# Optimization experiments

Hardware: AMD Instinct MI355X
Metric: run time of the kernel (lower is better)

## Reference

```python
import jax, jax.numpy as jnp
import numpy as np

B, L = 8, 896
D_MODEL, N_HEAD, D_HEAD, D_INNER = 320, 10, 32, 1280
LN_EPS = 1e-5


def layernorm(x, g, b):
    mu = jnp.mean(x, axis=-1, keepdims=True)
    var = jnp.mean(jnp.square(x - mu), axis=-1, keepdims=True)
    return (x - mu) * jax.lax.rsqrt(var + LN_EPS) * g + b


def setup_inputs() -> dict:
    key = jax.random.key(0)
    ks = jax.random.split(key, 8)
    w = lambda k, shape: (jax.random.normal(k, shape, jnp.float32) * 0.02)
    return {
        "Z": jax.random.normal(ks[0], (B, L, D_MODEL), jnp.float32),
        "D": jax.random.uniform(ks[1], (B, L, L), jnp.float32),  # nonneg sq-distance bias
        "new_mask": jnp.zeros((B, L, L), jnp.float32),           # additive mask (0 = keep)
        "mask": jnp.ones((B, L, L), jnp.float32),                # multiplicative validity mask
        "gamma": jnp.ones((4, 4), jnp.float32),
        "w_qkv": w(ks[2], (D_MODEL, 3 * D_MODEL)),
        "b_qkv": jnp.zeros((3 * D_MODEL,), jnp.float32),
        "w_o": w(ks[3], (D_MODEL, D_MODEL)),
        "ln1_g": jnp.ones((D_MODEL,), jnp.float32),
        "ln1_b": jnp.zeros((D_MODEL,), jnp.float32),
        "ln2_g": jnp.ones((D_MODEL,), jnp.float32),
        "ln2_b": jnp.zeros((D_MODEL,), jnp.float32),
        "w1": w(ks[4], (D_MODEL, D_INNER)),
        "b1": jnp.zeros((D_INNER,), jnp.float32),
        "w2": w(ks[5], (D_INNER, D_MODEL)),
        "b2": jnp.zeros((D_MODEL,), jnp.float32),
        "N": 128, "M": 256, "P": 512,
    }


def reference(Z, D, new_mask, mask, gamma, w_qkv, b_qkv, w_o,
              ln1_g, ln1_b, ln2_g, ln2_b, w1, b1, w2, b2, N, M, P):
    bsz, n_elem, _ = Z.shape
    sqrtd = np.sqrt(D_HEAD).astype(np.float32)

    # per-pair type bias: segment ids 0=atom,1=bond,2=triplet (use_quad=False)
    seg = jnp.concatenate([
        jnp.zeros((N,), jnp.int32),
        jnp.ones((M,), jnp.int32),
        jnp.full((P,), 2, jnp.int32),
    ])  # [L]
    gamma_mask = gamma[seg[:, None], seg[None, :]]  # [L, L]

    inp = Z
    Zn = layernorm(Z, ln1_g, ln1_b)
    qkv = (Zn @ w_qkv + b_qkv).reshape(bsz, n_elem, N_HEAD, 3 * D_HEAD)
    Z2, Z3, Z4 = jnp.split(qkv, 3, axis=3)  # each [b, L, h, d]

    # scores [b, h, n, m]
    scores = jnp.einsum('bnhd,bmhd->bhnm', Z3, Z4) / sqrtd
    W = -(gamma_mask[None] * D)[:, None] + scores + new_mask[:, None]
    W = jax.nn.softmax(W, axis=3) * mask[:, None]

    attn_out = jnp.einsum('bhnm,bmhd->bnhd', W, Z2).reshape(bsz, n_elem, D_MODEL)
    attn_out = jax.nn.leaky_relu(attn_out, 0.01) @ w_o  # o_net has no bias
    Z_res = attn_out + inp

    Zn2 = layernorm(Z_res, ln2_g, ln2_b)
    out = jax.nn.relu(Zn2 @ w1 + b1) @ w2 + b2 + Z_res
    return out
```

## Files before the change

kernel.cpp:

```cpp
#include <hip/hip_runtime.h>

#define BB 8
#define LLEN 896
#define DMODEL 320
#define NHEAD 10
#define DHEAD 32
#define DINNER 1280
#define ROWS (BB*LLEN)

typedef float f32x4 __attribute__((ext_vector_type(4)));
typedef float f32x16 __attribute__((ext_vector_type(16)));
typedef __bf16 bf16x8 __attribute__((ext_vector_type(8)));
typedef short s16x8 __attribute__((ext_vector_type(8)));

__device__ __forceinline__ float bf2f(unsigned short u) {
    union { unsigned int i; float f; } x;
    x.i = ((unsigned int)u) << 16;
    return x.f;
}
__device__ __forceinline__ unsigned short f2bf(float f) {
    unsigned int u = __float_as_uint(f);
    u += 0x7FFF + ((u >> 16) & 1);
    return (unsigned short)(u >> 16);
}

#define GLOAD16(g, l)                                                              \
    __builtin_amdgcn_global_load_lds(                                              \
        (const __attribute__((address_space(1))) void*)(g),                        \
        (__attribute__((address_space(3))) void*)(__attribute__((address_space(3))) char*)(l), \
        16, 0, 0)

__global__ __launch_bounds__(256) void transpose_bf16(const float* __restrict__ src,
                                                      unsigned short* __restrict__ dst,
                                                      int R, int C) {
    __shared__ float tile[32][33];
    int c0 = blockIdx.x * 32;
    int r0 = blockIdx.y * 32;
    int tx = threadIdx.x & 31, ty = threadIdx.x >> 5;
#pragma unroll
    for (int k = 0; k < 4; ++k) {
        int yy = ty + 8 * k;
        tile[yy][tx] = src[(size_t)(r0 + yy) * C + c0 + tx];
    }
    __syncthreads();
#pragma unroll
    for (int k = 0; k < 4; ++k) {
        int yy = ty + 8 * k;
        dst[(size_t)(c0 + yy) * R + r0 + tx] = f2bf(tile[tx][yy]);
    }
}

__global__ __launch_bounds__(256) void prepass(const float* __restrict__ D,
                                               const float* __restrict__ nm,
                                               const float* __restrict__ mk,
                                               const float* __restrict__ gamma,
                                               unsigned int* __restrict__ combo) {
    __shared__ unsigned int tile[32][33];
    int mt = blockIdx.x, m0 = mt * 32;
    int n0 = blockIdx.y * 32;
    int b = blockIdx.z;
    int sn = (n0 < 128) ? 0 : (n0 < 384) ? 1 : 2;
    int sm = (m0 < 128) ? 0 : (m0 < 384) ? 1 : 2;
    float g = gamma[sn * 4 + sm];
    int tx = threadIdx.x & 31, ty = threadIdx.x >> 5;
#pragma unroll
    for (int k = 0; k < 4; ++k) {
        int nl = ty + 8 * k;
        size_t idx = ((size_t)b * LLEN + n0 + nl) * LLEN + m0 + tx;
        float bias = -g * D[idx] + nm[idx];
        tile[nl][tx] = (unsigned int)f2bf(bias) | ((unsigned int)f2bf(mk[idx]) << 16);
    }
    __syncthreads();
#pragma unroll
    for (int k = 0; k < 4; ++k) {
        int nl = ty + 8 * k;
        combo[(((size_t)b * 28 + mt) * LLEN + n0 + nl) * 32 + tx] = tile[nl][tx];
    }
}

__global__ __launch_bounds__(256) void vt_kernel(const unsigned short* __restrict__ qkv,
                                                 unsigned short* __restrict__ Vt) {
    __shared__ unsigned short tile[32][33];
    int mt = blockIdx.x, h = blockIdx.y, b = blockIdx.z;
    int tx = threadIdx.x & 31, ty = threadIdx.x >> 5;
#pragma unroll
    for (int k = 0; k < 4; ++k) {
        int ml = ty + 8 * k;
        tile[ml][tx] = qkv[((size_t)(b * LLEN) + mt * 32 + ml) * 960 + h * 96 + tx];
    }
    __syncthreads();
#pragma unroll
    for (int k = 0; k < 4; ++k) {
        int d = ty + 8 * k;
        Vt[(((size_t)b * NHEAD + h) * 32 + d) * LLEN + mt * 32 + tx] = tile[tx][d];
    }
}

__global__ __launch_bounds__(320) void ln_kernel(const float* __restrict__ x,
                                                 const float* __restrict__ g,
                                                 const float* __restrict__ bia,
                                                 unsigned short* __restrict__ y) {
    int row = blockIdx.x;
    int t = threadIdx.x;
    float v = x[(size_t)row * DMODEL + t];
    float s = v;
#pragma unroll
    for (int o = 1; o < 64; o <<= 1) s += __shfl_xor(s, o, 64);
    __shared__ float red[10];
    int w = t >> 6;
    if ((t & 63) == 0) red[w] = s;
    __syncthreads();
    float mu = (red[0] + red[1] + red[2] + red[3] + red[4]) * (1.0f / DMODEL);
    float d = v - mu;
    float s2 = d * d;
#pragma unroll
    for (int o = 1; o < 64; o <<= 1) s2 += __shfl_xor(s2, o, 64);
    if ((t & 63) == 0) red[5 + w] = s2;
    __syncthreads();
    float var = (red[5] + red[6] + red[7] + red[8] + red[9]) * (1.0f / DMODEL);
    float inv = rsqrtf(var + 1e-5f);
    y[(size_t)row * DMODEL + t] = f2bf(d * inv * g[t] + bia[t]);
}

template <int EPI>
__global__ __launch_bounds__(256) void gemm_bt(const unsigned short* __restrict__ A,
                                               const unsigned short* __restrict__ BT,
                                               const float* __restrict__ bias,
                                               const float* __restrict__ resid,
                                               void* __restrict__ outv,
                                               int M, int N, int K) {
    __shared__ unsigned short As[128][64];
    __shared__ unsigned short Bs[64][64];
    int tid = threadIdx.x;
    int m0 = blockIdx.x * 128;
    int n0 = blockIdx.y * 64;
    int wid = tid >> 6, l = tid & 63;
    int wr = wid >> 1, wc = wid & 1;
    int lr = l & 15, lh = l >> 4;
    int srow = tid >> 3;
    int scol = (tid & 7) * 8;
    int wlds = (tid >> 6) * 1024;

    f32x4 acc[4][2];
#pragma unroll
    for (int mi = 0; mi < 4; ++mi)
#pragma unroll
        for (int ni = 0; ni < 2; ++ni) acc[mi][ni] = (f32x4){0.f, 0.f, 0.f, 0.f};

    for (int k0 = 0; k0 < K; k0 += 64) {
        __syncthreads();
#pragma unroll
        for (int i = 0; i < 4; ++i)
            GLOAD16(&A[(size_t)(m0 + i * 32 + srow) * K + k0 + scol],
                    (char*)&As[0][0] + i * 4096 + wlds);
#pragma unroll
        for (int i = 0; i < 2; ++i)
            GLOAD16(&BT[(size_t)(n0 + i * 32 + srow) * K + k0 + scol],
                    (char*)&Bs[0][0] + i * 4096 + wlds);
        __syncthreads();
#pragma unroll
        for (int kk = 0; kk < 2; ++kk) {
            bf16x8 b0 = *(const bf16x8*)&Bs[wc * 32 + lr][kk * 32 + lh * 8];
            bf16x8 b1 = *(const bf16x8*)&Bs[wc * 32 + 16 + lr][kk * 32 + lh * 8];
#pragma unroll
            for (int mi = 0; mi < 4; ++mi) {
                bf16x8 a = *(const bf16x8*)&As[wr * 64 + mi * 16 + lr][kk * 32 + lh * 8];
                acc[mi][0] = __builtin_amdgcn_mfma_f32_16x16x32_bf16(a, b0, acc[mi][0], 0, 0, 0);
                acc[mi][1] = __builtin_amdgcn_mfma_f32_16x16x32_bf16(a, b1, acc[mi][1], 0, 0, 0);
            }
        }
    }

    unsigned short* outb = (unsigned short*)outv;
    float* outf = (float*)outv;
#pragma unroll
    for (int mi = 0; mi < 4; ++mi)
#pragma unroll
        for (int ni = 0; ni < 2; ++ni) {
            int col = n0 + wc * 32 + ni * 16 + lr;
            float bv = (EPI != 1) ? bias[col] : 0.f;
#pragma unroll
            for (int j = 0; j < 4; ++j) {
                int row = m0 + wr * 64 + mi * 16 + lh * 4 + j;
                float v = acc[mi][ni][j];
                if (EPI == 0 || EPI == 2 || EPI == 3) v += bv;
                if (EPI == 2) v = fmaxf(v, 0.0f);
                if (EPI == 1 || EPI == 3) v += resid[(size_t)row * N + col];
                if (EPI == 0 || EPI == 2) outb[(size_t)row * N + col] = f2bf(v);
                else outf[(size_t)row * N + col] = v;
            }
        }
}

__global__ __launch_bounds__(320) void attn_mfma(const unsigned short* __restrict__ qkv,
                                                 const unsigned short* __restrict__ Vt,
                                                 const unsigned int* __restrict__ combo,
                                                 unsigned short* __restrict__ attn) {
    int tid = threadIdx.x;
    int h = blockIdx.y * 5 + (tid >> 6);
    int l = tid & 63;
    int c = l & 31;
    int hi = l >> 5;
    int nt = blockIdx.x % 28;
    int b = blockIdx.x / 28;
    int n0 = nt * 32;

    size_t qbase = ((size_t)(b * LLEN + n0 + c)) * 960 + h * 96 + 32 + hi * 8;
    bf16x8 qB0 = *(const bf16x8*)&qkv[qbase];
    bf16x8 qB1 = *(const bf16x8*)&qkv[qbase + 16];

    f32x16 oacc = {0.f,0.f,0.f,0.f,0.f,0.f,0.f,0.f,0.f,0.f,0.f,0.f,0.f,0.f,0.f,0.f};
    float lsum = 0.f;

    const unsigned int* cbase = combo + ((size_t)b * 28 * LLEN + n0 + c) * 32;
    size_t kbase = (size_t)b * LLEN * 960 + h * 96 + 64 + hi * 8;
    const unsigned short* vrow = Vt + (((size_t)b * NHEAD + h) * 32 + c) * LLEN;

    for (int mt = 0; mt < 28; ++mt) {
        size_t krow = kbase + (size_t)(mt * 32 + c) * 960;
        bf16x8 kA0 = *(const bf16x8*)&qkv[krow];
        bf16x8 kA1 = *(const bf16x8*)&qkv[krow + 16];
        f32x16 sacc = {0.f,0.f,0.f,0.f,0.f,0.f,0.f,0.f,0.f,0.f,0.f,0.f,0.f,0.f,0.f,0.f};
        sacc = __builtin_amdgcn_mfma_f32_32x32x16_bf16(kA0, qB0, sacc, 0, 0, 0);
        sacc = __builtin_amdgcn_mfma_f32_32x32x16_bf16(kA1, qB1, sacc, 0, 0, 0);

        const unsigned int* cp = cbase + (size_t)mt * (LLEN * 32);
        int4 x4[4];
#pragma unroll
        for (int g = 0; g < 4; ++g) x4[g] = *(const int4*)&cp[8 * g + 4 * hi];

        float p[16];
#pragma unroll
        for (int r = 0; r < 16; ++r) {
            unsigned int cm = ((const unsigned int*)x4)[(r >> 2) * 4 + (r & 3)];
            float bias = bf2f((unsigned short)(cm & 0xffffu));
            float mk = bf2f((unsigned short)(cm >> 16));
            float s = fmaf(sacc[r], 0.17677669529663687f, bias);
            float e = __expf(s);
            lsum += e;
            p[r] = e * mk;
        }

        unsigned int u[8], x[8];
#pragma unroll
        for (int j = 0; j < 8; ++j) {
            union { __bf16 h2[2]; unsigned int w; } pk;
            pk.h2[0] = (__bf16)p[2 * j];
            pk.h2[1] = (__bf16)p[2 * j + 1];
            u[j] = pk.w;
            x[j] = (unsigned int)__shfl_xor((int)u[j], 32, 64);
        }
        union { unsigned int w[4]; bf16x8 v; } a1, a2;
        if (hi == 0) {
            a1.w[0] = u[0]; a1.w[1] = u[1]; a1.w[2] = x[0]; a1.w[3] = x[1];
            a2.w[0] = u[4]; a2.w[1] = u[5]; a2.w[2] = x[4]; a2.w[3] = x[5];
        } else {
            a1.w[0] = x[2]; a1.w[1] = x[3]; a1.w[2] = u[2]; a1.w[3] = u[3];
            a2.w[0] = x[6]; a2.w[1] = x[7]; a2.w[2] = u[6]; a2.w[3] = u[7];
        }

        bf16x8 v1 = *(const bf16x8*)&vrow[mt * 32 + hi * 8];
        bf16x8 v2 = *(const bf16x8*)&vrow[mt * 32 + 16 + hi * 8];
        oacc = __builtin_amdgcn_mfma_f32_32x32x16_bf16(a1.v, v1, oacc, 0, 0, 0);
        oacc = __builtin_amdgcn_mfma_f32_32x32x16_bf16(a2.v, v2, oacc, 0, 0, 0);
    }

    lsum += __shfl_xor(lsum, 32, 64);
    float invs = 1.0f / lsum;
#pragma unroll
    for (int r = 0; r < 16; ++r) {
        int n = (r & 3) + 8 * (r >> 2) + 4 * hi;
        float o = oacc[r] * __shfl(invs, n, 64);
        o = (o >= 0.f) ? o : 0.01f * o;
        attn[((size_t)(b * LLEN + n0 + n)) * DMODEL + h * DHEAD + c] = f2bf(o);
    }
}

extern "C" void kernel_launch(void* const* d_in, const int* in_sizes, int n_in,
                              void* d_out, int out_size, void* d_ws, size_t ws_size,
                              hipStream_t stream) {
    const float* Z     = (const float*)d_in[0];
    const float* Dm    = (const float*)d_in[1];
    const float* nmask = (const float*)d_in[2];
    const float* mask  = (const float*)d_in[3];
    const float* gamma = (const float*)d_in[4];
    const float* w_qkv = (const float*)d_in[5];
    const float* b_qkv = (const float*)d_in[6];
    const float* w_o   = (const float*)d_in[7];
    const float* ln1g  = (const float*)d_in[8];
    const float* ln1b  = (const float*)d_in[9];
    const float* ln2g  = (const float*)d_in[10];
    const float* ln2b  = (const float*)d_in[11];
    const float* w1    = (const float*)d_in[12];
    const float* b1    = (const float*)d_in[13];
    const float* w2    = (const float*)d_in[14];
    const float* b2    = (const float*)d_in[15];

    char* ws = (char*)d_ws;
    unsigned short* Zn    = (unsigned short*)(ws + 0);
    unsigned short* qkv   = (unsigned short*)(ws + 4587520);
    unsigned short* attn  = (unsigned short*)(ws + 18350080);
    float*          Zres  = (float*)(ws + 22937600);
    unsigned short* Zn2   = (unsigned short*)(ws + 32112640);
    unsigned short* Hbuf  = (unsigned short*)(ws + 36700160);
    unsigned short* wqkvT = (unsigned short*)(ws + 55050240);
    unsigned short* woT   = (unsigned short*)(ws + 55664640);
    unsigned short* w1T   = (unsigned short*)(ws + 55869440);
    unsigned short* w2T   = (unsigned short*)(ws + 56688640);
    unsigned int*   combo = (unsigned int*)(ws + 57507840);
    unsigned short* Vtb   = (unsigned short*)(ws + 83197952);

    transpose_bf16<<<dim3(960 / 32, 320 / 32), 256, 0, stream>>>(w_qkv, wqkvT, 320, 960);
    transpose_bf16<<<dim3(320 / 32, 320 / 32), 256, 0, stream>>>(w_o, woT, 320, 320);
    transpose_bf16<<<dim3(1280 / 32, 320 / 32), 256, 0, stream>>>(w1, w1T, 320, 1280);
    transpose_bf16<<<dim3(320 / 32, 1280 / 32), 256, 0, stream>>>(w2, w2T, 1280, 320);

    prepass<<<dim3(28, 28, 8), 256, 0, stream>>>(Dm, nmask, mask, gamma, combo);

    ln_kernel<<<ROWS, 320, 0, stream>>>(Z, ln1g, ln1b, Zn);

    gemm_bt<0><<<dim3(ROWS / 128, 960 / 64), 256, 0, stream>>>(Zn, wqkvT, b_qkv, nullptr,
                                                               (void*)qkv, ROWS, 960, 320);

    vt_kernel<<<dim3(28, NHEAD, BB), 256, 0, stream>>>(qkv, Vtb);

    attn_mfma<<<dim3(BB * 28, 2), 320, 0, stream>>>(qkv, Vtb, combo, attn);

    gemm_bt<1><<<dim3(ROWS / 128, 320 / 64), 256, 0, stream>>>(attn, woT, nullptr, Z,
                                                               (void*)Zres, ROWS, 320, 320);

    ln_kernel<<<ROWS, 320, 0, stream>>>(Zres, ln2g, ln2b, Zn2);

    gemm_bt<2><<<dim3(ROWS / 128, 1280 / 64), 256, 0, stream>>>(Zn2, w1T, b1, nullptr,
                                                                (void*)Hbuf, ROWS, 1280, 320);

    gemm_bt<3><<<dim3(ROWS / 128, 320 / 64), 256, 0, stream>>>(Hbuf, w2T, b2, Zres,
                                                               d_out, ROWS, 320, 1280);
}
```

Before: 308.6 us.

## Swizzle GEMM LDS tiles and double-buffer attention loads in registers

The GEMM stages A and B tiles into LDS through a XOR-swizzled chunk layout, so MFMA operand reads spread across banks instead of conflicting. The attention loop is restructured into a two-stage register double buffer: K, V and the combined bias/mask for the next key tile are loaded while the current tile is computed. This hides global load latency behind MFMA and exp work at the cost of extra registers, which may reduce occupancy; the final iteration issues a redundant prefetch of tile 0.

```diff
diff --git a/kernel.cpp b/kernel.cpp
--- a/kernel.cpp
+++ b/kernel.cpp
@@ -11,7 +11,6 @@
 typedef float f32x4 __attribute__((ext_vector_type(4)));
 typedef float f32x16 __attribute__((ext_vector_type(16)));
 typedef __bf16 bf16x8 __attribute__((ext_vector_type(8)));
-typedef short s16x8 __attribute__((ext_vector_type(8)));
 
 __device__ __forceinline__ float bf2f(unsigned short u) {
     union { unsigned int i; float f; } x;
@@ -138,8 +137,7 @@
     int wr = wid >> 1, wc = wid & 1;
     int lr = l & 15, lh = l >> 4;
     int srow = tid >> 3;
-    int scol = (tid & 7) * 8;
-    int wlds = (tid >> 6) * 1024;
+    int sslot = (tid & 7) ^ (srow & 7);
 
     f32x4 acc[4][2];
 #pragma unroll
@@ -151,20 +149,22 @@
         __syncthreads();
 #pragma unroll
         for (int i = 0; i < 4; ++i)
-            GLOAD16(&A[(size_t)(m0 + i * 32 + srow) * K + k0 + scol],
-                    (char*)&As[0][0] + i * 4096 + wlds);
+            GLOAD16(&A[(size_t)(m0 + i * 32 + srow) * K + k0 + sslot * 8],
+                    (char*)&As[0][0] + i * 4096 + tid * 16);
 #pragma unroll
         for (int i = 0; i < 2; ++i)
-            GLOAD16(&BT[(size_t)(n0 + i * 32 + srow) * K + k0 + scol],
-                    (char*)&Bs[0][0] + i * 4096 + wlds);
+            GLOAD16(&BT[(size_t)(n0 + i * 32 + srow) * K + k0 + sslot * 8],
+                    (char*)&Bs[0][0] + i * 4096 + tid * 16);
         __syncthreads();
 #pragma unroll
         for (int kk = 0; kk < 2; ++kk) {
-            bf16x8 b0 = *(const bf16x8*)&Bs[wc * 32 + lr][kk * 32 + lh * 8];
-            bf16x8 b1 = *(const bf16x8*)&Bs[wc * 32 + 16 + lr][kk * 32 + lh * 8];
+            int gch = kk * 4 + lh;
+            int sl = gch ^ (lr & 7);
+            bf16x8 b0 = *(const bf16x8*)&Bs[wc * 32 + lr][sl * 8];
+            bf16x8 b1 = *(const bf16x8*)&Bs[wc * 32 + 16 + lr][sl * 8];
 #pragma unroll
             for (int mi = 0; mi < 4; ++mi) {
-                bf16x8 a = *(const bf16x8*)&As[wr * 64 + mi * 16 + lr][kk * 32 + lh * 8];
+                bf16x8 a = *(const bf16x8*)&As[wr * 64 + mi * 16 + lr][sl * 8];
                 acc[mi][0] = __builtin_amdgcn_mfma_f32_16x16x32_bf16(a, b0, acc[mi][0], 0, 0, 0);
                 acc[mi][1] = __builtin_amdgcn_mfma_f32_16x16x32_bf16(a, b1, acc[mi][1], 0, 0, 0);
             }
@@ -216,53 +216,67 @@
     size_t kbase = (size_t)b * LLEN * 960 + h * 96 + 64 + hi * 8;
     const unsigned short* vrow = Vt + (((size_t)b * NHEAD + h) * 32 + c) * LLEN;
 
-    for (int mt = 0; mt < 28; ++mt) {
-        size_t krow = kbase + (size_t)(mt * 32 + c) * 960;
-        bf16x8 kA0 = *(const bf16x8*)&qkv[krow];
-        bf16x8 kA1 = *(const bf16x8*)&qkv[krow + 16];
-        f32x16 sacc = {0.f,0.f,0.f,0.f,0.f,0.f,0.f,0.f,0.f,0.f,0.f,0.f,0.f,0.f,0.f,0.f};
-        sacc = __builtin_amdgcn_mfma_f32_32x32x16_bf16(kA0, qB0, sacc, 0, 0, 0);
-        sacc = __builtin_amdgcn_mfma_f32_32x32x16_bf16(kA1, qB1, sacc, 0, 0, 0);
-
-        const unsigned int* cp = cbase + (size_t)mt * (LLEN * 32);
-        int4 x4[4];
-#pragma unroll
-        for (int g = 0; g < 4; ++g) x4[g] = *(const int4*)&cp[8 * g + 4 * hi];
-
-        float p[16];
-#pragma unroll
-        for (int r = 0; r < 16; ++r) {
-            unsigned int cm = ((const unsigned int*)x4)[(r >> 2) * 4 + (r & 3)];
-            float bias = bf2f((unsigned short)(cm & 0xffffu));
-            float mk = bf2f((unsigned short)(cm >> 16));
-            float s = fmaf(sacc[r], 0.17677669529663687f, bias);
-            float e = __expf(s);
-            lsum += e;
-            p[r] = e * mk;
-        }
-
-        unsigned int u[8], x[8];
-#pragma unroll
-        for (int j = 0; j < 8; ++j) {
-            union { __bf16 h2[2]; unsigned int w; } pk;
-            pk.h2[0] = (__bf16)p[2 * j];
-            pk.h2[1] = (__bf16)p[2 * j + 1];
-            u[j] = pk.w;
-            x[j] = (unsigned int)__shfl_xor((int)u[j], 32, 64);
-        }
-        union { unsigned int w[4]; bf16x8 v; } a1, a2;
-        if (hi == 0) {
-            a1.w[0] = u[0]; a1.w[1] = u[1]; a1.w[2] = x[0]; a1.w[3] = x[1];
-            a2.w[0] = u[4]; a2.w[1] = u[5]; a2.w[2] = x[4]; a2.w[3] = x[5];
-        } else {
-            a1.w[0] = x[2]; a1.w[1] = x[3]; a1.w[2] = u[2]; a1.w[3] = u[3];
-            a2.w[0] = x[6]; a2.w[1] = x[7]; a2.w[2] = u[6]; a2.w[3] = u[7];
-        }
-
-        bf16x8 v1 = *(const bf16x8*)&vrow[mt * 32 + hi * 8];
-        bf16x8 v2 = *(const bf16x8*)&vrow[mt * 32 + 16 + hi * 8];
-        oacc = __builtin_amdgcn_mfma_f32_32x32x16_bf16(a1.v, v1, oacc, 0, 0, 0);
-        oacc = __builtin_amdgcn_mfma_f32_32x32x16_bf16(a2.v, v2, oacc, 0, 0, 0);
+#define ALOAD(mt, K0, K1, V1_, V2_, X4)                                     \
+    {                                                                       \
+        size_t krow = kbase + (size_t)((mt) * 32 + c) * 960;                \
+        K0 = *(const bf16x8*)&qkv[krow];                                    \
+        K1 = *(const bf16x8*)&qkv[krow + 16];                               \
+        V1_ = *(const bf16x8*)&vrow[(mt) * 32 + hi * 8];                    \
+        V2_ = *(const bf16x8*)&vrow[(mt) * 32 + 16 + hi * 8];               \
+        const unsigned int* cp = cbase + (size_t)(mt) * (LLEN * 32);        \
+        X4[0] = *(const int4*)&cp[4 * hi];                                  \
+        X4[1] = *(const int4*)&cp[8 + 4 * hi];                              \
+        X4[2] = *(const int4*)&cp[16 + 4 * hi];                             \
+        X4[3] = *(const int4*)&cp[24 + 4 * hi];                             \
+    }
+
+#define ACOMPUTE(K0, K1, V1_, V2_, X4)                                                \
+    {                                                                                 \
+        f32x16 sacc = {0.f,0.f,0.f,0.f,0.f,0.f,0.f,0.f,0.f,0.f,0.f,0.f,0.f,0.f,0.f,0.f}; \
+        sacc = __builtin_amdgcn_mfma_f32_32x32x16_bf16(K0, qB0, sacc, 0, 0, 0);       \
+        sacc = __builtin_amdgcn_mfma_f32_32x32x16_bf16(K1, qB1, sacc, 0, 0, 0);       \
+        float p[16];                                                                  \
+        _Pragma("unroll")                                                             \
+        for (int r = 0; r < 16; ++r) {                                                \
+            unsigned int cm = ((const unsigned int*)X4)[r];                           \
+            float bias = bf2f((unsigned short)(cm & 0xffffu));                        \
+            float mk = bf2f((unsigned short)(cm >> 16));                              \
+            float s = fmaf(sacc[r], 0.17677669529663687f, bias);                      \
+            float e = __expf(s);                                                      \
+            lsum += e;                                                                \
+            p[r] = e * mk;                                                            \
+        }                                                                             \
+        unsigned int u[8], x[8];                                                      \
+        _Pragma("unroll")                                                             \
+        for (int j = 0; j < 8; ++j) {                                                 \
+            union { __bf16 h2[2]; unsigned int w; } pk;                               \
+            pk.h2[0] = (__bf16)p[2 * j];                                              \
+            pk.h2[1] = (__bf16)p[2 * j + 1];                                          \
+            u[j] = pk.w;                                                              \
+            x[j] = (unsigned int)__shfl_xor((int)u[j], 32, 64);                       \
+        }                                                                             \
+        union { unsigned int w[4]; bf16x8 v; } a1, a2;                                \
+        if (hi == 0) {                                                                \
+            a1.w[0] = u[0]; a1.w[1] = u[1]; a1.w[2] = x[0]; a1.w[3] = x[1];           \
+            a2.w[0] = u[4]; a2.w[1] = u[5]; a2.w[2] = x[4]; a2.w[3] = x[5];           \
+        } else {                                                                      \
+            a1.w[0] = x[2]; a1.w[1] = x[3]; a1.w[2] = u[2]; a1.w[3] = u[3];           \
+            a2.w[0] = x[6]; a2.w[1] = x[7]; a2.w[2] = u[6]; a2.w[3] = u[7];           \
+        }                                                                             \
+        oacc = __builtin_amdgcn_mfma_f32_32x32x16_bf16(a1.v, V1_, oacc, 0, 0, 0);     \
+        oacc = __builtin_amdgcn_mfma_f32_32x32x16_bf16(a2.v, V2_, oacc, 0, 0, 0);     \
+    }
+
+    bf16x8 k0A, k1A, v1A, v2A; int4 xA[4];
+    bf16x8 k0B, k1B, v1B, v2B; int4 xB[4];
+    ALOAD(0, k0A, k1A, v1A, v2A, xA);
+#pragma unroll 1
+    for (int mt = 0; mt < 28; mt += 2) {
+        ALOAD(mt + 1, k0B, k1B, v1B, v2B, xB);
+        ACOMPUTE(k0A, k1A, v1A, v2A, xA);
+        int nx = (mt + 2 < 28) ? mt + 2 : 0;
+        ALOAD(nx, k0A, k1A, v1A, v2A, xA);
+        ACOMPUTE(k0B, k1B, v1B, v2B, xB);
     }
 
     lsum += __shfl_xor(lsum, 32, 64);
@@ -274,6 +288,8 @@
         o = (o >= 0.f) ? o : 0.01f * o;
         attn[((size_t)(b * LLEN + n0 + n)) * DMODEL + h * DHEAD + c] = f2bf(o);
     }
+#undef ALOAD
+#undef ACOMPUTE
 }
 
 extern "C" void kernel_launch(void* const* d_in, const int* in_sizes, int n_in,
```

After: 303.0 us. Within noise of the previous version (-1.8%).
